# Kernel optimization log

Measured on AMD Instinct MI355X. Metric: run time of the kernel, lower is better.

The kernel has to match this reference:

```python
import jax, jax.numpy as jnp
import numpy as np

D = 1024
N_HEAD = 16
D_HEAD = D // N_HEAD
B, S = 4, 2048
EPS = 1e-6


def rmsnorm(x, w):
    # x: [..., d_head]
    return x / jnp.sqrt(jnp.mean(x * x, axis=-1, keepdims=True) + EPS) * w


def setup_inputs() -> dict:
    key = jax.random.key(0)
    ks = jax.random.split(key, 6)
    x = jax.random.normal(ks[0], (B, S, D), dtype=jnp.float32)
    # causal mask: True means masked (upper triangle above diagonal)
    mask = jnp.triu(jnp.ones((S, S), dtype=bool), k=1)
    scale = 1.0 / np.sqrt(D)
    W_qkv = jax.random.normal(ks[1], (D, 3 * D), dtype=jnp.float32) * scale
    b_qkv = jnp.zeros((3 * D,), dtype=jnp.float32)
    W_o = jax.random.normal(ks[2], (D, D), dtype=jnp.float32) * scale
    b_o = jnp.zeros((D,), dtype=jnp.float32)
    wq = jnp.ones((D_HEAD,), dtype=jnp.float32)
    wk = jnp.ones((D_HEAD,), dtype=jnp.float32)
    return {"x": x, "mask": mask, "W_qkv": W_qkv, "b_qkv": b_qkv,
            "W_o": W_o, "b_o": b_o, "wq": wq, "wk": wk}


def reference(x, mask, W_qkv, b_qkv, W_o, b_o, wq, wk):
    b, s, d = x.shape
    qkv = x @ W_qkv + b_qkv  # [b,s,3d]
    q, k, v = jnp.split(qkv, 3, axis=-1)
    q = q.reshape(b, s, N_HEAD, D_HEAD)
    k = k.reshape(b, s, N_HEAD, D_HEAD)
    v = v.reshape(b, s, N_HEAD, D_HEAD)
    q = rmsnorm(q, wq)
    k = rmsnorm(k, wk)
    # NOTE: no 1/sqrt(d_head) scaling, faithful to the source
    attn = jnp.einsum('bqhd,bkhd->bhqk', q, k)
    attn = jnp.where(mask[None, None, :, :], -jnp.inf, attn)
    attn = jax.nn.softmax(attn, axis=-1)
    z = jnp.einsum('bhqk,bkhd->bqhd', attn, v).reshape(b, s, d)
    return z @ W_o + b_o
```

## Files before the change

### kernel.cpp

```cpp
#include <hip/hip_runtime.h>
#include <cmath>

typedef _Float16 half_t;
typedef _Float16 half8 __attribute__((ext_vector_type(8)));
typedef _Float16 half4v __attribute__((ext_vector_type(4)));
typedef float float4v __attribute__((ext_vector_type(4)));

#define LOG2E 1.44269504088896340736f

#define GLDS16(g, l)                                                                   \
    __builtin_amdgcn_global_load_lds((const __attribute__((address_space(1))) void*)(g), \
                                     (__attribute__((address_space(3))) void*)(l), 16, 0, 0)

#define BAR_LGKM() __asm__ volatile("s_waitcnt lgkmcnt(0)\n\ts_barrier" ::: "memory")
#define BAR_VM(n)  __asm__ volatile("s_waitcnt vmcnt(" #n ")\n\ts_barrier" ::: "memory")

__global__ void cast_f32_f16(const float* __restrict__ in, half_t* __restrict__ out, int n) {
    int i = (blockIdx.x * blockDim.x + threadIdx.x) * 4;
    if (i >= n) return;
    float4 v = *(const float4*)(in + i);
    half4v o;
    o[0] = (half_t)v.x; o[1] = (half_t)v.y; o[2] = (half_t)v.z; o[3] = (half_t)v.w;
    *(half4v*)(out + i) = o;
}

__global__ void transpose_cast(const float* __restrict__ in, half_t* __restrict__ out, int R, int C) {
    __shared__ float tile[32][33];
    int c0 = blockIdx.x * 32, r0 = blockIdx.y * 32;
    int tx = threadIdx.x, ty = threadIdx.y;
    for (int p = 0; p < 4; p++) {
        int r = r0 + ty + p * 8;
        tile[ty + p * 8][tx] = in[(size_t)r * C + c0 + tx];
    }
    __syncthreads();
    for (int p = 0; p < 4; p++) {
        int c = c0 + ty + p * 8;
        out[(size_t)c * R + r0 + tx] = (half_t)tile[tx][ty + p * 8];
    }
}

__global__ __launch_bounds__(512, 2) void gemm_qkv(
    const half_t* __restrict__ A,
    const half_t* __restrict__ Bt,
    const float* __restrict__ bias,
    const float* __restrict__ wq, const float* __restrict__ wk,
    half_t* __restrict__ Qh, half_t* __restrict__ Kh, half_t* __restrict__ Vt,
    int M, int N, int K)
{
    __shared__ __align__(16) half_t As[2][2][128 * 64];
    __shared__ __align__(16) half_t Bs[2][2][256 * 32];

    int t = threadIdx.x;
    int lane = t & 63, w = t >> 6;
    int lrow = lane & 15, quad = lane >> 4;
    int wm = w >> 2, wn = w & 3;

    int cpx = gridDim.x >> 3;
    int bid = blockIdx.x;
    int wg = (bid & 7) * cpx + (bid >> 3);
    int nbn = N >> 8;
    int mb = wg / nbn, nb = wg % nbn;
    int m0 = mb << 8, n0 = nb << 8;

    int ar = t >> 3;
    int ac = (t & 7) ^ (ar & 7);
    const half_t* gAbase = A + (size_t)(m0 + ar) * K + ac * 8;
    int br = t >> 2;
    int bc = ((t & 3) - (t >> 3)) & 3;
    const half_t* gBbase = Bt + (size_t)(n0 + br) * K + bc * 8;

    auto stageA = [&](int buf, int a, int T) {
        const half_t* s = gAbase + (size_t)a * 128 * K + T * 64;
        GLDS16(s,                  &As[buf][a][w * 512]);
        GLDS16(s + (size_t)64 * K, &As[buf][a][4096 + w * 512]);
    };
    auto stageB = [&](int buf, int kh, int T) {
        const half_t* s = gBbase + T * 64 + kh * 32;
        GLDS16(s,                   &Bs[buf][kh][w * 512]);
        GLDS16(s + (size_t)128 * K, &Bs[buf][kh][4096 + w * 512]);
    };

    int sw = lrow & 7;
    int cx0 = ((0 + quad) ^ sw) * 8;
    int cx1 = ((4 + quad) ^ sw) * 8;
    int posq = (quad + (lrow >> 1)) & 3;
    int aoffs = (wm * 64 + lrow) * 64;
    int boffs = (wn * 64 + lrow) * 32 + posq * 8;

    half8 af[4][2];
    half8 b0[4], b1[4];
    float4v acc[2][4][4] = {};

    auto loadA = [&](int buf, int a) {
        #pragma unroll
        for (int mi = 0; mi < 4; mi++) {
            af[mi][0] = *(const half8*)(&As[buf][a][aoffs + mi * 1024 + cx0]);
            af[mi][1] = *(const half8*)(&As[buf][a][aoffs + mi * 1024 + cx1]);
        }
    };
    auto loadB = [&](int buf, int kh, half8* bf) {
        #pragma unroll
        for (int ni = 0; ni < 4; ni++)
            bf[ni] = *(const half8*)(&Bs[buf][kh][boffs + ni * 512]);
    };

#define PHASE_OPEN()                                               \
    do {                                                           \
        __asm__ volatile("s_barrier" ::: "memory");                \
        __asm__ volatile("s_waitcnt lgkmcnt(0)" ::: "memory");     \
        __builtin_amdgcn_sched_barrier(0);                         \
        __builtin_amdgcn_s_setprio(1);                             \
    } while (0)
#define PHASE_CLOSE()                                              \
    do {                                                           \
        __builtin_amdgcn_s_setprio(0);                             \
        __builtin_amdgcn_sched_barrier(0);                         \
        __asm__ volatile("s_barrier" ::: "memory");                \
    } while (0)
#define MFMA16(A_, KH_, BF_)                                                           \
    do {                                                                               \
        _Pragma("unroll")                                                              \
        for (int mi = 0; mi < 4; mi++) {                                               \
            _Pragma("unroll")                                                          \
            for (int ni = 0; ni < 4; ni++)                                             \
                acc[A_][mi][ni] = __builtin_amdgcn_mfma_f32_16x16x32_f16(              \
                    af[mi][KH_], BF_[ni], acc[A_][mi][ni], 0, 0, 0);                   \
        }                                                                              \
    } while (0)

    int nk = K >> 6;

    stageA(0, 0, 0); stageB(0, 0, 0); stageA(0, 1, 0); stageB(0, 1, 0);
    stageA(1, 0, 1); stageB(1, 0, 1); stageA(1, 1, 1);
    __asm__ volatile("s_waitcnt vmcnt(6)" ::: "memory");
    __asm__ volatile("s_barrier" ::: "memory");

    for (int T = 0; T < nk; T++) {
        int buf = T & 1, nbuf = buf ^ 1;
        loadA(buf, 0);
        loadB(buf, 0, b0);
        if (T + 1 < nk) stageB(nbuf, 1, T + 1);
        __asm__ volatile("s_waitcnt lgkmcnt(8)" ::: "memory");
        PHASE_OPEN();
        MFMA16(0, 0, b0);
        PHASE_CLOSE();
        loadB(buf, 1, b1);
        if (T + 2 < nk) stageA(buf, 0, T + 2);
        PHASE_OPEN();
        MFMA16(0, 1, b1);
        PHASE_CLOSE();
        loadA(buf, 1);
        if (T + 2 < nk) stageB(buf, 0, T + 2);
        PHASE_OPEN();
        MFMA16(1, 1, b1);
        PHASE_CLOSE();
        if (T + 2 < nk) stageA(buf, 1, T + 2);
        PHASE_OPEN();
        MFMA16(1, 0, b0);
        __builtin_amdgcn_s_setprio(0);
        __builtin_amdgcn_sched_barrier(0);
        if (T + 2 < nk) {
            __asm__ volatile("s_waitcnt vmcnt(6)" ::: "memory");
        } else if (T + 1 < nk) {
            __asm__ volatile("s_waitcnt vmcnt(0)" ::: "memory");
        }
        __asm__ volatile("s_barrier" ::: "memory");
    }

    int nglob = n0 + wn * 64;
    if (nglob < 2048) {
        int isK = nglob >> 10;
        int h = (nglob >> 6) & 15;
        const float* wv = isK ? wk : wq;
        half_t* dst = isK ? Kh : Qh;
        float post = isK ? 1.0f : LOG2E;
        #pragma unroll
        for (int a = 0; a < 2; a++) {
            #pragma unroll
            for (int mi = 0; mi < 4; mi++) {
                #pragma unroll
                for (int r = 0; r < 4; r++) {
                    int gr = m0 + a * 128 + wm * 64 + mi * 16 + quad * 4 + r;
                    float v[4]; float ss = 0.f;
                    #pragma unroll
                    for (int ni = 0; ni < 4; ni++) {
                        v[ni] = acc[a][mi][ni][r] + bias[nglob + ni * 16 + lrow];
                        ss += v[ni] * v[ni];
                    }
                    ss += __shfl_xor(ss, 1);
                    ss += __shfl_xor(ss, 2);
                    ss += __shfl_xor(ss, 4);
                    ss += __shfl_xor(ss, 8);
                    float rr = rsqrtf(ss * (1.0f / 64.0f) + 1e-6f) * post;
                    int bb = gr >> 11, s = gr & 2047;
                    size_t rowbase = ((size_t)((bb * 16 + h) * 2048 + s)) * 64;
                    #pragma unroll
                    for (int ni = 0; ni < 4; ni++) {
                        int d = ni * 16 + lrow;
                        dst[rowbase + d] = (half_t)(v[ni] * rr * wv[d]);
                    }
                }
            }
        }
    } else {
        #pragma unroll
        for (int a = 0; a < 2; a++) {
            #pragma unroll
            for (int mi = 0; mi < 4; mi++) {
                int gr = m0 + a * 128 + wm * 64 + mi * 16 + quad * 4;
                int bb = gr >> 11, s = gr & 2047;
                #pragma unroll
                for (int ni = 0; ni < 4; ni++) {
                    int dg = nglob + ni * 16 + lrow - 2048;
                    float bv = bias[nglob + ni * 16 + lrow];
                    half4v oh;
                    #pragma unroll
                    for (int r = 0; r < 4; r++) oh[r] = (half_t)(acc[a][mi][ni][r] + bv);
                    *(half4v*)(Vt + ((size_t)((bb * 16 + (dg >> 6)) * 64 + (dg & 63))) * 2048 + s) = oh;
                }
            }
        }
    }
#undef PHASE_OPEN
#undef PHASE_CLOSE
#undef MFMA16
}

template <int MODE>
__global__ __launch_bounds__(256, 3) void gemm_f16(
    const half_t* __restrict__ A,
    const half_t* __restrict__ Bt,
    const float* __restrict__ bias,
    void* __restrict__ Cout,
    int M, int N, int K,
    const float* __restrict__ wq, const float* __restrict__ wk,
    half_t* __restrict__ Qh, half_t* __restrict__ Kh)
{
    __shared__ __align__(16) half_t As[3][128 * 32];
    __shared__ __align__(16) half_t Bs[3][128 * 32];
    int t = threadIdx.x;
    int lane = t & 63, w = t >> 6;
    int m0 = blockIdx.x * 128, n0 = blockIdx.y * 128;
    int wm = (w >> 1) * 64, wn = (w & 1) * 64;
    int lrow = lane & 15, quad = lane >> 4;

    int lc = ((t & 3) - (t >> 3)) & 3;
    const half_t* gA = A  + (size_t)(m0 + (t >> 2)) * K + lc * 8;
    const half_t* gB = Bt + (size_t)(n0 + (t >> 2)) * K + lc * 8;
    half_t* ldsA[3] = { &As[0][w * 512], &As[1][w * 512], &As[2][w * 512] };
    half_t* ldsB[3] = { &Bs[0][w * 512], &Bs[1][w * 512], &Bs[2][w * 512] };

    int posq = (quad + (lrow >> 1)) & 3;

    float4v acc[4][4] = {};

    GLDS16(gA,                       ldsA[0]);
    GLDS16(gA + (size_t)64 * K,      ldsA[0] + 2048);
    GLDS16(gB,                       ldsB[0]);
    GLDS16(gB + (size_t)64 * K,      ldsB[0] + 2048);
    GLDS16(gA + 32,                  ldsA[1]);
    GLDS16(gA + (size_t)64 * K + 32, ldsA[1] + 2048);
    GLDS16(gB + 32,                  ldsB[1]);
    GLDS16(gB + (size_t)64 * K + 32, ldsB[1] + 2048);

    int nk = K >> 5;
    for (int ki = 0; ki < nk; ki++) {
        int cur = ki % 3, pre = (ki + 2) % 3;
        BAR_LGKM();
        if (ki + 2 < nk) {
            int kp = (ki + 2) << 5;
            GLDS16(gA + kp,                  ldsA[pre]);
            GLDS16(gA + (size_t)64 * K + kp, ldsA[pre] + 2048);
            GLDS16(gB + kp,                  ldsB[pre]);
            GLDS16(gB + (size_t)64 * K + kp, ldsB[pre] + 2048);
            BAR_VM(8);
        } else if (ki + 1 < nk) {
            BAR_VM(4);
        } else {
            BAR_VM(0);
        }
        half8 af[4], bf[4];
        for (int i = 0; i < 4; i++) af[i] = *(const half8*)(&As[cur][(wm + i * 16 + lrow) * 32 + posq * 8]);
        for (int i = 0; i < 4; i++) bf[i] = *(const half8*)(&Bs[cur][(wn + i * 16 + lrow) * 32 + posq * 8]);
        for (int mi = 0; mi < 4; mi++)
            for (int ni = 0; ni < 4; ni++)
                acc[mi][ni] = __builtin_amdgcn_mfma_f32_16x16x32_f16(af[mi], bf[ni], acc[mi][ni], 0, 0, 0);
    }

    if (MODE == 0) {
        float* out = (float*)Cout;
        for (int mi = 0; mi < 4; mi++)
            for (int ni = 0; ni < 4; ni++)
                for (int r = 0; r < 4; r++) {
                    int gr = m0 + wm + mi * 16 + quad * 4 + r;
                    int gc = n0 + wn + ni * 16 + lrow;
                    out[(size_t)gr * N + gc] = acc[mi][ni][r] + bias[gc];
                }
    } else {
        int nglob = n0 + wn;
        if (nglob < 2048) {
            int isK = nglob >> 10;
            int h = (nglob >> 6) & 15;
            const float* wv = isK ? wk : wq;
            half_t* dst = isK ? Kh : Qh;
            float post = isK ? 1.0f : LOG2E;
            for (int mi = 0; mi < 4; mi++)
                for (int r = 0; r < 4; r++) {
                    int gr = m0 + wm + mi * 16 + quad * 4 + r;
                    float v[4]; float ss = 0.f;
                    for (int ni = 0; ni < 4; ni++) {
                        v[ni] = acc[mi][ni][r] + bias[nglob + ni * 16 + lrow];
                        ss += v[ni] * v[ni];
                    }
                    ss += __shfl_xor(ss, 1);
                    ss += __shfl_xor(ss, 2);
                    ss += __shfl_xor(ss, 4);
                    ss += __shfl_xor(ss, 8);
                    float rr = rsqrtf(ss * (1.0f / 64.0f) + 1e-6f) * post;
                    int bb = gr >> 11, s = gr & 2047;
                    size_t rowbase = ((size_t)((bb * 16 + h) * 2048 + s)) * 64;
                    for (int ni = 0; ni < 4; ni++) {
                        int d = ni * 16 + lrow;
                        dst[rowbase + d] = (half_t)(v[ni] * rr * wv[d]);
                    }
                }
        } else {
            half_t* Vt = (half_t*)Cout;
            for (int mi = 0; mi < 4; mi++) {
                int gr = m0 + wm + mi * 16 + quad * 4;
                int bb = gr >> 11, s = gr & 2047;
                for (int ni = 0; ni < 4; ni++) {
                    int dg = nglob + ni * 16 + lrow - 2048;
                    float bv = bias[nglob + ni * 16 + lrow];
                    half4v oh;
                    for (int r = 0; r < 4; r++) oh[r] = (half_t)(acc[mi][ni][r] + bv);
                    *(half4v*)(Vt + ((size_t)((bb * 16 + (dg >> 6)) * 64 + (dg & 63))) * 2048 + s) = oh;
                }
            }
        }
    }
}

__global__ __launch_bounds__(512, 4) void attn(
    const half_t* __restrict__ Qh, const half_t* __restrict__ Kh, const half_t* __restrict__ Vt,
    half_t* __restrict__ Z)
{
    __shared__ __align__(16) half_t Ks[2][128 * 64];
    __shared__ __align__(16) half_t Vs[2][64 * 128];
    __shared__ __align__(16) half_t Ps[8][16 * 64];

    int bh = blockIdx.x;
    int b = bh >> 4, h = bh & 15;
    int t = threadIdx.x, lane = t & 63, w = t >> 6;
    int lrow = lane & 15, quad = lane >> 4;

    int scc = (lane & 7) ^ ((lane >> 3) & 7);
    const half_t* gK0 = Kh + ((size_t)bh * 2048 + w * 16 + (lane >> 3)) * 64 + scc * 8;
    int vr0 = w * 8 + (lane >> 4);
    int vc0 = (lane & 15) ^ (lane >> 4);
    int vc1 = (lane & 15) ^ ((lane >> 4) + 4);
    const half_t* gV0 = Vt + ((size_t)bh * 64 + vr0) * 2048 + vc0 * 8;
    const half_t* gV1 = Vt + ((size_t)bh * 64 + vr0 + 4) * 2048 + vc1 * 8;
    half_t* ldsK[2] = { &Ks[0][w * 1024], &Ks[1][w * 1024] };
    half_t* ldsV[2] = { &Vs[0][w * 1024], &Vs[1][w * 1024] };

    int sw = lrow & 7;
    int cA = (quad ^ sw) * 8;
    int cB = ((quad + 4) ^ sw) * 8;
    half_t* PsW = &Ps[w][lrow * 64];

    for (int pass = 0; pass < 2; pass++) {
        int qt = pass ? (15 - (int)blockIdx.y) : (int)blockIdx.y;
        int q0w = qt * 128 + w * 16;

        const half_t* Qbase = Qh + ((size_t)bh * 2048 + q0w + lrow) * 64;
        half8 qf0 = *(const half8*)(Qbase + quad * 8);
        half8 qf1 = *(const half8*)(Qbase + 32 + quad * 8);

        float4v ot[4] = {};
        float m = -__builtin_inff(), l = 0.f;

        int nt = qt + 1;
        __syncthreads();
        GLDS16(gK0,       ldsK[0]);
        GLDS16(gK0 + 512, ldsK[0] + 512);
        GLDS16(gV0,       ldsV[0]);
        GLDS16(gV1,       ldsV[0] + 512);

        for (int kt = 0; kt < nt; kt++) {
            int cur = kt & 1, nxt = cur ^ 1;
            int kb = kt * 128;
            BAR_LGKM();
            if (kt + 1 < nt) {
                size_t ko = (size_t)(kb + 128);
                GLDS16(gK0 + ko * 64,       ldsK[nxt]);
                GLDS16(gK0 + ko * 64 + 512, ldsK[nxt] + 512);
                GLDS16(gV0 + ko,            ldsV[nxt]);
                GLDS16(gV1 + ko,            ldsV[nxt] + 512);
                BAR_VM(4);
            } else {
                BAR_VM(0);
            }

            float4v st[8];
            for (int f = 0; f < 8; f++) {
                float4v z = {};
                const half_t* kr = &Ks[cur][(f * 16 + lrow) * 64];
                half8 k0 = *(const half8*)(kr + cA);
                half8 k1 = *(const half8*)(kr + cB);
                z = __builtin_amdgcn_mfma_f32_16x16x32_f16(k0, qf0, z, 0, 0, 0);
                z = __builtin_amdgcn_mfma_f32_16x16x32_f16(k1, qf1, z, 0, 0, 0);
                st[f] = z;
            }
            if (kb + 127 > q0w) {
                int qabs = q0w + lrow;
                for (int f = 0; f < 8; f++)
                    for (int r = 0; r < 4; r++) {
                        int key = kb + f * 16 + quad * 4 + r;
                        if (key > qabs) st[f][r] = -__builtin_inff();
                    }
            }
            float tm = st[0][0];
            for (int f = 0; f < 8; f++)
                for (int r = 0; r < 4; r++) tm = fmaxf(tm, st[f][r]);
            tm = fmaxf(tm, __shfl_xor(tm, 16));
            tm = fmaxf(tm, __shfl_xor(tm, 32));
            float mn = fmaxf(m, tm);
            float alpha = __builtin_amdgcn_exp2f(m - mn);
            m = mn;
            float rs = 0.f;
            uint2 pw1[4];
            for (int f = 0; f < 8; f++) {
                float p0 = __builtin_amdgcn_exp2f(st[f][0] - mn);
                float p1 = __builtin_amdgcn_exp2f(st[f][1] - mn);
                float p2 = __builtin_amdgcn_exp2f(st[f][2] - mn);
                float p3 = __builtin_amdgcn_exp2f(st[f][3] - mn);
                rs += (p0 + p1) + (p2 + p3);
                uint2 pw;
                pw.x = __builtin_bit_cast(unsigned, __builtin_amdgcn_cvt_pkrtz(p0, p1));
                pw.y = __builtin_bit_cast(unsigned, __builtin_amdgcn_cvt_pkrtz(p2, p3));
                if (f < 4) {
                    int cc = (2 * f + (quad >> 1)) ^ sw;
                    *(uint2*)(PsW + cc * 8 + (quad & 1) * 4) = pw;
                } else {
                    pw1[f - 4] = pw;
                }
            }
            rs += __shfl_xor(rs, 16);
            rs += __shfl_xor(rs, 32);
            l = l * alpha + rs;
            for (int f2 = 0; f2 < 4; f2++)
                for (int r = 0; r < 4; r++) ot[f2][r] *= alpha;

            __asm__ volatile("s_waitcnt lgkmcnt(0)" ::: "memory");
            half8 p0v = *(const half8*)(PsW + cA);
            half8 p1v = *(const half8*)(PsW + cB);
            for (int f2 = 0; f2 < 4; f2++) {
                int row = f2 * 16 + lrow;
                half8 v0 = *(const half8*)(&Vs[cur][row * 128 + ((quad ^ sw)) * 8]);
                half8 v1 = *(const half8*)(&Vs[cur][row * 128 + (((4 + quad) ^ sw)) * 8]);
                ot[f2] = __builtin_amdgcn_mfma_f32_16x16x32_f16(v0, p0v, ot[f2], 0, 0, 0);
                ot[f2] = __builtin_amdgcn_mfma_f32_16x16x32_f16(v1, p1v, ot[f2], 0, 0, 0);
            }
            for (int f = 0; f < 4; f++) {
                int cc = (2 * f + (quad >> 1)) ^ sw;
                *(uint2*)(PsW + cc * 8 + (quad & 1) * 4) = pw1[f];
            }
            __asm__ volatile("s_waitcnt lgkmcnt(0)" ::: "memory");
            half8 p2v = *(const half8*)(PsW + cA);
            half8 p3v = *(const half8*)(PsW + cB);
            for (int f2 = 0; f2 < 4; f2++) {
                int row = f2 * 16 + lrow;
                half8 v2 = *(const half8*)(&Vs[cur][row * 128 + (((8 + quad) ^ sw)) * 8]);
                half8 v3 = *(const half8*)(&Vs[cur][row * 128 + (((12 + quad) ^ sw)) * 8]);
                ot[f2] = __builtin_amdgcn_mfma_f32_16x16x32_f16(v2, p2v, ot[f2], 0, 0, 0);
                ot[f2] = __builtin_amdgcn_mfma_f32_16x16x32_f16(v3, p3v, ot[f2], 0, 0, 0);
            }
        }

        float inv = 1.0f / l;
        size_t base = ((size_t)(b * 2048) + q0w + lrow) * 1024 + h * 64;
        for (int f2 = 0; f2 < 4; f2++) {
            half4v oh;
            for (int r = 0; r < 4; r++) oh[r] = (half_t)(ot[f2][r] * inv);
            *(half4v*)(Z + base + f2 * 16 + quad * 4) = oh;
        }
    }
}

extern "C" void kernel_launch(void* const* d_in, const int* in_sizes, int n_in,
                              void* d_out, int out_size, void* d_ws, size_t ws_size,
                              hipStream_t stream)
{
    const float* x     = (const float*)d_in[0];
    const float* W_qkv = (const float*)d_in[2];
    const float* b_qkv = (const float*)d_in[3];
    const float* W_o   = (const float*)d_in[4];
    const float* b_o   = (const float*)d_in[5];
    const float* wq    = (const float*)d_in[6];
    const float* wk    = (const float*)d_in[7];
    float* out = (float*)d_out;

    char* ws = (char*)d_ws;
    half_t* xh   = (half_t*)(ws);
    half_t* Wqt  = (half_t*)(ws + (16ull << 20));
    half_t* Wot  = (half_t*)(ws + (22ull << 20));
    half_t* Qh   = (half_t*)(ws + (40ull << 20));
    half_t* Kh   = (half_t*)(ws + (56ull << 20));
    half_t* Vt   = (half_t*)(ws + (72ull << 20));
    half_t* zh   = xh;

    cast_f32_f16<<<8192, 256, 0, stream>>>(x, xh, 8192 * 1024);
    transpose_cast<<<dim3(96, 32), dim3(32, 8), 0, stream>>>(W_qkv, Wqt, 1024, 3072);
    transpose_cast<<<dim3(32, 32), dim3(32, 8), 0, stream>>>(W_o, Wot, 1024, 1024);
    gemm_qkv<<<384, 512, 0, stream>>>(xh, Wqt, b_qkv, wq, wk, Qh, Kh, Vt, 8192, 3072, 1024);
    attn<<<dim3(64, 8), 512, 0, stream>>>(Qh, Kh, Vt, zh);
    gemm_f16<0><<<dim3(64, 8), 256, 0, stream>>>(zh, Wot, b_o, out, 8192, 1024, 1024,
                                                 nullptr, nullptr, nullptr, nullptr);
}
```

Measured before the change: 276.9 us.

## Restructure QKV GEMM main loop into two-phase pipeline with register double-buffering

Replaces the four-phase-per-tile QKV GEMM loop with two phases per k-tile. It prefetches the next tile's A and B fragments into alternate register sets (afA/afB, bX/bY) while the MFMAs for the current tile run. Each phase issues 32 MFMAs covering both k-halves, and the global-to-LDS staging is regrouped so that A and B are staged together with vmcnt(4) waits. The goal is fewer barriers per tile and better hiding of LDS-read latency behind MFMAs. The cost is more vector registers, which may hurt occupancy. The unroll-by-two loop also assumes nk is even.

```diff
diff --git a/kernel.cpp b/kernel.cpp
--- a/kernel.cpp
+++ b/kernel.cpp
@@ -87,84 +87,84 @@
     int aoffs = (wm * 64 + lrow) * 64;
     int boffs = (wn * 64 + lrow) * 32 + posq * 8;
 
-    half8 af[4][2];
-    half8 b0[4], b1[4];
+    half8 afA[4][2], afB[4][2];
+    half8 bX0[4], bX1[4], bY0[4], bY1[4];
     float4v acc[2][4][4] = {};
 
-    auto loadA = [&](int buf, int a) {
+    auto loadAf = [&](int buf, int a, half8 (&dst)[4][2]) {
         #pragma unroll
         for (int mi = 0; mi < 4; mi++) {
-            af[mi][0] = *(const half8*)(&As[buf][a][aoffs + mi * 1024 + cx0]);
-            af[mi][1] = *(const half8*)(&As[buf][a][aoffs + mi * 1024 + cx1]);
+            dst[mi][0] = *(const half8*)(&As[buf][a][aoffs + mi * 1024 + cx0]);
+            dst[mi][1] = *(const half8*)(&As[buf][a][aoffs + mi * 1024 + cx1]);
         }
     };
-    auto loadB = [&](int buf, int kh, half8* bf) {
+    auto loadBf = [&](int buf, int kh, half8 (&dst)[4]) {
         #pragma unroll
         for (int ni = 0; ni < 4; ni++)
-            bf[ni] = *(const half8*)(&Bs[buf][kh][boffs + ni * 512]);
+            dst[ni] = *(const half8*)(&Bs[buf][kh][boffs + ni * 512]);
     };
 
-#define PHASE_OPEN()                                               \
-    do {                                                           \
-        __asm__ volatile("s_barrier" ::: "memory");                \
-        __asm__ volatile("s_waitcnt lgkmcnt(0)" ::: "memory");     \
-        __builtin_amdgcn_sched_barrier(0);                         \
-        __builtin_amdgcn_s_setprio(1);                             \
+#define MFMA32(AF, B0A, B1A, AI)                                                  \
+    do { _Pragma("unroll")                                                        \
+        for (int mi = 0; mi < 4; mi++) { _Pragma("unroll")                        \
+            for (int ni = 0; ni < 4; ni++) {                                      \
+                acc[AI][mi][ni] = __builtin_amdgcn_mfma_f32_16x16x32_f16(         \
+                    AF[mi][0], B0A[ni], acc[AI][mi][ni], 0, 0, 0);                \
+                acc[AI][mi][ni] = __builtin_amdgcn_mfma_f32_16x16x32_f16(         \
+                    AF[mi][1], B1A[ni], acc[AI][mi][ni], 0, 0, 0);                \
+            } } } while (0)
+
+#define TILE_BODY(T_, BC0, BC1, BN0, BN1)                                         \
+    do {                                                                          \
+        const int Tb = (T_);                                                      \
+        const int bufb = Tb & 1, nbufb = bufb ^ 1;                                \
+         \
+        __asm__ volatile("s_waitcnt lgkmcnt(0)" ::: "memory");                    \
+        __builtin_amdgcn_sched_barrier(0);                                        \
+        __asm__ volatile("s_barrier" ::: "memory");                               \
+        loadAf(bufb, 1, afB);                                                     \
+        if (Tb + 2 < nk) { stageA(bufb, 0, Tb + 2); stageB(bufb, 0, Tb + 2); }    \
+        __builtin_amdgcn_sched_barrier(0);                                        \
+        __builtin_amdgcn_s_setprio(1);                                            \
+        MFMA32(afA, BC0, BC1, 0);                                                 \
+        __builtin_amdgcn_s_setprio(0);                                            \
+        __builtin_amdgcn_sched_barrier(0);                                        \
+        if (Tb + 2 < nk) { __asm__ volatile("s_waitcnt vmcnt(4)" ::: "memory"); } \
+        else             { __asm__ volatile("s_waitcnt vmcnt(0)" ::: "memory"); } \
+        __asm__ volatile("s_barrier" ::: "memory");                               \
+          \
+        __asm__ volatile("s_waitcnt lgkmcnt(0)" ::: "memory");                    \
+        __builtin_amdgcn_sched_barrier(0);                                        \
+        __asm__ volatile("s_barrier" ::: "memory");                               \
+        if (Tb + 1 < nk) {                                                        \
+            loadAf(nbufb, 0, afA);                                                \
+            loadBf(nbufb, 0, BN0);                                                \
+            loadBf(nbufb, 1, BN1);                                                \
+        }                                                                         \
+        if (Tb + 2 < nk) { stageA(bufb, 1, Tb + 2); stageB(bufb, 1, Tb + 2); }    \
+        __builtin_amdgcn_sched_barrier(0);                                        \
+        __builtin_amdgcn_s_setprio(1);                                            \
+        MFMA32(afB, BC0, BC1, 1);                                                 \
+        __builtin_amdgcn_s_setprio(0);                                            \
+        __builtin_amdgcn_sched_barrier(0);                                        \
+        if (Tb + 2 < nk) { __asm__ volatile("s_waitcnt vmcnt(4)" ::: "memory"); } \
+        else             { __asm__ volatile("s_waitcnt vmcnt(0)" ::: "memory"); } \
+        __asm__ volatile("s_barrier" ::: "memory");                               \
     } while (0)
-#define PHASE_CLOSE()                                              \
-    do {                                                           \
-        __builtin_amdgcn_s_setprio(0);                             \
-        __builtin_amdgcn_sched_barrier(0);                         \
-        __asm__ volatile("s_barrier" ::: "memory");                \
-    } while (0)
-#define MFMA16(A_, KH_, BF_)                                                           \
-    do {                                                                               \
-        _Pragma("unroll")                                                              \
-        for (int mi = 0; mi < 4; mi++) {                                               \
-            _Pragma("unroll")                                                          \
-            for (int ni = 0; ni < 4; ni++)                                             \
-                acc[A_][mi][ni] = __builtin_amdgcn_mfma_f32_16x16x32_f16(              \
-                    af[mi][KH_], BF_[ni], acc[A_][mi][ni], 0, 0, 0);                   \
-        }                                                                              \
-    } while (0)
 
     int nk = K >> 6;
 
     stageA(0, 0, 0); stageB(0, 0, 0); stageA(0, 1, 0); stageB(0, 1, 0);
-    stageA(1, 0, 1); stageB(1, 0, 1); stageA(1, 1, 1);
-    __asm__ volatile("s_waitcnt vmcnt(6)" ::: "memory");
+    stageA(1, 0, 1); stageB(1, 0, 1); stageA(1, 1, 1); stageB(1, 1, 1);
+    __asm__ volatile("s_waitcnt vmcnt(8)" ::: "memory");
     __asm__ volatile("s_barrier" ::: "memory");
-
-    for (int T = 0; T < nk; T++) {
-        int buf = T & 1, nbuf = buf ^ 1;
-        loadA(buf, 0);
-        loadB(buf, 0, b0);
-        if (T + 1 < nk) stageB(nbuf, 1, T + 1);
-        __asm__ volatile("s_waitcnt lgkmcnt(8)" ::: "memory");
-        PHASE_OPEN();
-        MFMA16(0, 0, b0);
-        PHASE_CLOSE();
-        loadB(buf, 1, b1);
-        if (T + 2 < nk) stageA(buf, 0, T + 2);
-        PHASE_OPEN();
-        MFMA16(0, 1, b1);
-        PHASE_CLOSE();
-        loadA(buf, 1);
-        if (T + 2 < nk) stageB(buf, 0, T + 2);
-        PHASE_OPEN();
-        MFMA16(1, 1, b1);
-        PHASE_CLOSE();
-        if (T + 2 < nk) stageA(buf, 1, T + 2);
-        PHASE_OPEN();
-        MFMA16(1, 0, b0);
-        __builtin_amdgcn_s_setprio(0);
-        __builtin_amdgcn_sched_barrier(0);
-        if (T + 2 < nk) {
-            __asm__ volatile("s_waitcnt vmcnt(6)" ::: "memory");
-        } else if (T + 1 < nk) {
-            __asm__ volatile("s_waitcnt vmcnt(0)" ::: "memory");
-        }
-        __asm__ volatile("s_barrier" ::: "memory");
+    loadAf(0, 0, afA);
+    loadBf(0, 0, bX0);
+    loadBf(0, 1, bX1);
+
+    for (int T0 = 0; T0 < nk; T0 += 2) {
+        TILE_BODY(T0,     bX0, bX1, bY0, bY1);
+        TILE_BODY(T0 + 1, bY0, bY1, bX0, bX1);
     }
 
     int nglob = n0 + wn * 64;
@@ -221,9 +221,8 @@
             }
         }
     }
-#undef PHASE_OPEN
-#undef PHASE_CLOSE
-#undef MFMA16
+#undef TILE_BODY
+#undef MFMA32
 }
 
 template <int MODE>
```

Result: slower. 383.9 us (+38.6%).

## Software-pipeline LDS fragment loads one phase ahead in fused QKV GEMM

Applied to the files above, without the earlier changes.

Restructures the QKV GEMM main loop so that the A and B fragment reads from shared memory for the next MFMA phase are issued before the current phase's MFMAs, with double-buffered register fragments (af0/af1). The first fragments of the next K-tile are prefetched during the last phases. Each phase now uses a single barrier, where before it had open and close barriers, and the global-to-LDS stage order changes. The intent is to hide LDS latency behind MFMA work and cut barrier count. It raises register pressure, and the waitcnt and barrier accounting has to stay exactly right to avoid races.

```diff
diff --git a/kernel.cpp b/kernel.cpp
--- a/kernel.cpp
+++ b/kernel.cpp
@@ -87,84 +87,95 @@
     int aoffs = (wm * 64 + lrow) * 64;
     int boffs = (wn * 64 + lrow) * 32 + posq * 8;
 
-    half8 af[4][2];
+    half8 af0[4], af1[4];
     half8 b0[4], b1[4];
     float4v acc[2][4][4] = {};
 
-    auto loadA = [&](int buf, int a) {
+    auto loadAk = [&](int buf, int a, int cx, half8 (&dst)[4]) {
         #pragma unroll
-        for (int mi = 0; mi < 4; mi++) {
-            af[mi][0] = *(const half8*)(&As[buf][a][aoffs + mi * 1024 + cx0]);
-            af[mi][1] = *(const half8*)(&As[buf][a][aoffs + mi * 1024 + cx1]);
-        }
+        for (int mi = 0; mi < 4; mi++)
+            dst[mi] = *(const half8*)(&As[buf][a][aoffs + mi * 1024 + cx]);
     };
-    auto loadB = [&](int buf, int kh, half8* bf) {
+    auto loadBf = [&](int buf, int kh, half8 (&dst)[4]) {
         #pragma unroll
         for (int ni = 0; ni < 4; ni++)
-            bf[ni] = *(const half8*)(&Bs[buf][kh][boffs + ni * 512]);
+            dst[ni] = *(const half8*)(&Bs[buf][kh][boffs + ni * 512]);
     };
 
-#define PHASE_OPEN()                                               \
+#define MFMA16(AF, BF, AI)                                                        \
+    do { _Pragma("unroll")                                                        \
+        for (int mi = 0; mi < 4; mi++) { _Pragma("unroll")                        \
+            for (int ni = 0; ni < 4; ni++)                                        \
+                acc[AI][mi][ni] = __builtin_amdgcn_mfma_f32_16x16x32_f16(         \
+                    AF[mi], BF[ni], acc[AI][mi][ni], 0, 0, 0);                    \
+        } } while (0)
+
+#define PH_TOP()                                                   \
     do {                                                           \
-        __asm__ volatile("s_barrier" ::: "memory");                \
         __asm__ volatile("s_waitcnt lgkmcnt(0)" ::: "memory");     \
         __builtin_amdgcn_sched_barrier(0);                         \
-        __builtin_amdgcn_s_setprio(1);                             \
     } while (0)
-#define PHASE_CLOSE()                                              \
-    do {                                                           \
-        __builtin_amdgcn_s_setprio(0);                             \
-        __builtin_amdgcn_sched_barrier(0);                         \
-        __asm__ volatile("s_barrier" ::: "memory");                \
+#define PH_BOT(STG)                                                               \
+    do {                                                                          \
+        __builtin_amdgcn_sched_barrier(0);                                        \
+        if (STG) { __asm__ volatile("s_waitcnt vmcnt(6)" ::: "memory"); }         \
+        else     { __asm__ volatile("s_waitcnt vmcnt(0)" ::: "memory"); }         \
+        __asm__ volatile("s_barrier" ::: "memory");                               \
     } while (0)
-#define MFMA16(A_, KH_, BF_)                                                           \
-    do {                                                                               \
-        _Pragma("unroll")                                                              \
-        for (int mi = 0; mi < 4; mi++) {                                               \
-            _Pragma("unroll")                                                          \
-            for (int ni = 0; ni < 4; ni++)                                             \
-                acc[A_][mi][ni] = __builtin_amdgcn_mfma_f32_16x16x32_f16(              \
-                    af[mi][KH_], BF_[ni], acc[A_][mi][ni], 0, 0, 0);                   \
-        }                                                                              \
-    } while (0)
 
     int nk = K >> 6;
 
-    stageA(0, 0, 0); stageB(0, 0, 0); stageA(0, 1, 0); stageB(0, 1, 0);
-    stageA(1, 0, 1); stageB(1, 0, 1); stageA(1, 1, 1);
-    __asm__ volatile("s_waitcnt vmcnt(6)" ::: "memory");
+    stageB(0, 0, 0); stageB(0, 1, 0); stageA(0, 0, 0); stageA(0, 1, 0);
+    stageB(1, 0, 1); stageB(1, 1, 1); stageA(1, 0, 1); stageA(1, 1, 1);
+    __asm__ volatile("s_waitcnt vmcnt(8)" ::: "memory");
+    __asm__ volatile("s_barrier" ::: "memory");
+    loadAk(0, 0, cx0, af0);
+    loadBf(0, 0, b0);
+    __asm__ volatile("s_waitcnt lgkmcnt(0)" ::: "memory");
     __asm__ volatile("s_barrier" ::: "memory");
 
     for (int T = 0; T < nk; T++) {
         int buf = T & 1, nbuf = buf ^ 1;
-        loadA(buf, 0);
-        loadB(buf, 0, b0);
-        if (T + 1 < nk) stageB(nbuf, 1, T + 1);
-        __asm__ volatile("s_waitcnt lgkmcnt(8)" ::: "memory");
-        PHASE_OPEN();
-        MFMA16(0, 0, b0);
-        PHASE_CLOSE();
-        loadB(buf, 1, b1);
-        if (T + 2 < nk) stageA(buf, 0, T + 2);
-        PHASE_OPEN();
-        MFMA16(0, 1, b1);
-        PHASE_CLOSE();
-        loadA(buf, 1);
-        if (T + 2 < nk) stageB(buf, 0, T + 2);
-        PHASE_OPEN();
-        MFMA16(1, 1, b1);
-        PHASE_CLOSE();
-        if (T + 2 < nk) stageA(buf, 1, T + 2);
-        PHASE_OPEN();
-        MFMA16(1, 0, b0);
+        bool stg = (T + 2 < nk);
+        bool rdn = (T + 1 < nk);
+
+        PH_TOP();
+        loadAk(buf, 1, cx0, af1);
+        loadBf(buf, 1, b1);
+        if (stg) stageB(buf, 0, T + 2);
+        __builtin_amdgcn_sched_barrier(0);
+        __builtin_amdgcn_s_setprio(1);
+        MFMA16(af0, b0, 0);
         __builtin_amdgcn_s_setprio(0);
+        PH_BOT(stg);
+
+        PH_TOP();
+        loadAk(buf, 0, cx1, af0);
+        if (stg) stageB(buf, 1, T + 2);
         __builtin_amdgcn_sched_barrier(0);
-        if (T + 2 < nk) {
-            __asm__ volatile("s_waitcnt vmcnt(6)" ::: "memory");
-        } else if (T + 1 < nk) {
-            __asm__ volatile("s_waitcnt vmcnt(0)" ::: "memory");
-        }
-        __asm__ volatile("s_barrier" ::: "memory");
+        __builtin_amdgcn_s_setprio(1);
+        MFMA16(af1, b0, 1);
+        __builtin_amdgcn_s_setprio(0);
+        PH_BOT(stg);
+
+        PH_TOP();
+        loadAk(buf, 1, cx1, af1);
+        if (rdn) loadBf(nbuf, 0, b0);
+        if (stg) stageA(buf, 0, T + 2);
+        __builtin_amdgcn_sched_barrier(0);
+        __builtin_amdgcn_s_setprio(1);
+        MFMA16(af0, b1, 0);
+        __builtin_amdgcn_s_setprio(0);
+        PH_BOT(stg);
+
+        PH_TOP();
+        if (rdn) loadAk(nbuf, 0, cx0, af0);
+        if (stg) stageA(buf, 1, T + 2);
+        __builtin_amdgcn_sched_barrier(0);
+        __builtin_amdgcn_s_setprio(1);
+        MFMA16(af1, b1, 1);
+        __builtin_amdgcn_s_setprio(0);
+        PH_BOT(stg);
     }
 
     int nglob = n0 + wn * 64;
@@ -221,8 +232,8 @@
             }
         }
     }
-#undef PHASE_OPEN
-#undef PHASE_CLOSE
+#undef PH_TOP
+#undef PH_BOT
 #undef MFMA16
 }
 
```

Measured after the change: 273.3 us. No clear change (-1.3%).
